# Optimization experiments

Hardware: AMD Instinct MI355X
Metric: run time of the kernel (lower is better)

The kernel has to match this reference:

```python
import jax, jax.numpy as jnp
import numpy as np

HIDDEN = 2048
HEADS = 16
HEAD_DIM = HIDDEN // HEADS  # 128
B, S = 2, 2048


def setup_inputs() -> dict:
    key = jax.random.key(0)
    ks = jax.random.split(key, 9)
    s_in = 1.0 / np.sqrt(HIDDEN)
    return {
        "X": jax.random.normal(ks[0], (B, S, HIDDEN), dtype=jnp.float32),
        "attention_mask": jnp.ones((B, S, S), dtype=jnp.int32),
        "Wq": jax.random.uniform(ks[1], (HIDDEN, HIDDEN), jnp.float32, -s_in, s_in),
        "bq": jax.random.uniform(ks[2], (HIDDEN,), jnp.float32, -s_in, s_in),
        "Wk": jax.random.uniform(ks[3], (HIDDEN, HEAD_DIM), jnp.float32, -s_in, s_in),
        "bk": jax.random.uniform(ks[4], (HEAD_DIM,), jnp.float32, -s_in, s_in),
        "Wv": jax.random.uniform(ks[5], (HIDDEN, HEAD_DIM), jnp.float32, -s_in, s_in),
        "bv": jax.random.uniform(ks[6], (HEAD_DIM,), jnp.float32, -s_in, s_in),
        "Wo": jax.random.uniform(ks[7], (HIDDEN, HIDDEN), jnp.float32, -s_in, s_in),
        "bo": jax.random.uniform(ks[8], (HIDDEN,), jnp.float32, -s_in, s_in),
    }


def reference(X, attention_mask, Wq, bq, Wk, bk, Wv, bv, Wo, bo):
    b, s, _ = X.shape
    # Projections
    Q = X @ Wq + bq                      # (B, S, H*D)
    K = X @ Wk + bk                      # (B, S, D)  shared across heads (MQA)
    V = X @ Wv + bv                      # (B, S, D)
    Q = Q.reshape(b, s, HEADS, HEAD_DIM).transpose(0, 2, 1, 3)  # (B, H, S, D)
    scale = 1.0 / jnp.sqrt(jnp.float32(HEAD_DIM))
    # QK^T with shared K head
    scores = jnp.einsum('bhqd,bkd->bhqk', Q, K) * scale          # (B, H, S, S)
    scores = jnp.where(attention_mask[:, None, :, :] == 0, -jnp.inf, scores)
    attn = jax.nn.softmax(scores, axis=-1)
    # dropout_rate = 0.0 (eval) -> identity
    out = jnp.einsum('bhqk,bkd->bhqd', attn, V)                  # (B, H, S, D)
    out = out.transpose(0, 2, 1, 3).reshape(b, s, HIDDEN)        # (B, S, hidden)
    return out @ Wo + bo
```

## Files before the change

### kernel.cpp

```cpp
#include <hip/hip_runtime.h>
#include <cstdint>
#include <cstddef>

#define HIDDEN 2048
#define HEADS 16
#define HD 128
#define BSZ 2
#define SEQ 2048
#define MTOT (BSZ * SEQ)
#define NQKV (HIDDEN + 2 * HD)
#define SL2E 0.12751743f

typedef unsigned short ushort_t;
typedef __attribute__((ext_vector_type(8))) __bf16 bf16x8;
typedef __attribute__((ext_vector_type(4))) float f32x4;

typedef __attribute__((address_space(3))) unsigned int as3_u32;
typedef __attribute__((address_space(1))) const unsigned int as1_u32;

__device__ __forceinline__ ushort_t f2bf(float x) {
  union { float f; unsigned u; } v; v.f = x;
  unsigned r = v.u + 0x7fffu + ((v.u >> 16) & 1u);
  return (ushort_t)(r >> 16);
}
__device__ __forceinline__ ushort_t f2bf_trunc(float x) {
  union { float f; unsigned u; } v; v.f = x;
  return (ushort_t)(v.u >> 16);
}

__device__ __forceinline__ void gld16(const void* g, void* lds) {
  __builtin_amdgcn_global_load_lds((as1_u32*)g, (as3_u32*)lds, 16, 0, 0);
}

__global__ __launch_bounds__(256) void cvt_bf16_kernel(
    const float* __restrict__ in, ushort_t* __restrict__ out, int n4) {
  int i = blockIdx.x * 256 + threadIdx.x;
  if (i >= n4) return;
  float4 v = ((const float4*)in)[i];
  ushort4 o;
  o.x = f2bf(v.x); o.y = f2bf(v.y); o.z = f2bf(v.z); o.w = f2bf(v.w);
  ((ushort4*)out)[i] = o;
}

__global__ __launch_bounds__(256) void cvtT_qkv_kernel(
    const float* __restrict__ Wq, const float* __restrict__ Wk,
    const float* __restrict__ Wv, ushort_t* __restrict__ WT) {
  __shared__ float tile[32][36];
  const int t = threadIdx.x;
  const int nb = blockIdx.x * 32, kb = blockIdx.y * 32;
  const float* W; int N, nc; float scale;
  if (nb < HIDDEN)            { W = Wq; N = HIDDEN; nc = nb;               scale = SL2E; }
  else if (nb < HIDDEN + HD)  { W = Wk; N = HD;     nc = nb - HIDDEN;      scale = 1.f; }
  else                        { W = Wv; N = HD;     nc = nb - HIDDEN - HD; scale = 1.f; }
  {
    int row = t >> 3, c4 = (t & 7) << 2;
    float4 v = *(const float4*)(W + (size_t)(kb + row) * N + nc + c4);
    tile[row][c4] = v.x * scale; tile[row][c4 + 1] = v.y * scale;
    tile[row][c4 + 2] = v.z * scale; tile[row][c4 + 3] = v.w * scale;
  }
  __syncthreads();
  {
    int nl = t >> 3, k4 = (t & 7) << 2;
    ushort4 o;
    o.x = f2bf(tile[k4 + 0][nl]); o.y = f2bf(tile[k4 + 1][nl]);
    o.z = f2bf(tile[k4 + 2][nl]); o.w = f2bf(tile[k4 + 3][nl]);
    *(ushort4*)(WT + (size_t)(nb + nl) * HIDDEN + kb + k4) = o;
  }
}

__global__ __launch_bounds__(256) void cvtT_kernel(
    const float* __restrict__ W, ushort_t* __restrict__ WT, int K, int N) {
  __shared__ float tile[32][36];
  const int t = threadIdx.x;
  const int kb = blockIdx.y * 32, nb = blockIdx.x * 32;
  {
    int row = t >> 3, c4 = (t & 7) << 2;
    float4 v = *(const float4*)(W + (size_t)(kb + row) * N + nb + c4);
    tile[row][c4] = v.x; tile[row][c4 + 1] = v.y;
    tile[row][c4 + 2] = v.z; tile[row][c4 + 3] = v.w;
  }
  __syncthreads();
  {
    int nl = t >> 3, k4 = (t & 7) << 2;
    ushort4 o;
    o.x = f2bf(tile[k4 + 0][nl]); o.y = f2bf(tile[k4 + 1][nl]);
    o.z = f2bf(tile[k4 + 2][nl]); o.w = f2bf(tile[k4 + 3][nl]);
    *(ushort4*)(WT + (size_t)(nb + nl) * K + kb + k4) = o;
  }
}

__global__ __launch_bounds__(256) void transpose_v_kernel(
    const ushort_t* __restrict__ Vin, ushort_t* __restrict__ Vt) {
  __shared__ ushort_t tile[32][40];
  const int t = threadIdx.x;
  const int rb = blockIdx.x * 32, cb = blockIdx.y * 32;
  {
    int row = t >> 3, c4 = (t & 7) << 2;
    ushort4 v = *(const ushort4*)(Vin + (size_t)(rb + row) * NQKV + cb + c4);
    tile[row][c4] = v.x; tile[row][c4 + 1] = v.y;
    tile[row][c4 + 2] = v.z; tile[row][c4 + 3] = v.w;
  }
  __syncthreads();
  {
    int dl = t >> 3, r4 = (t & 7) << 2;
    ushort4 o;
    o.x = tile[r4 + 0][dl]; o.y = tile[r4 + 1][dl];
    o.z = tile[r4 + 2][dl]; o.w = tile[r4 + 3][dl];
    *(ushort4*)(Vt + (size_t)(cb + dl) * MTOT + rb + r4) = o;
  }
}

__global__ void concat_bias_kernel(const float* __restrict__ bq,
                                   const float* __restrict__ bk,
                                   const float* __restrict__ bv,
                                   float* __restrict__ o) {
  int i = blockIdx.x * 256 + threadIdx.x;
  if (i >= NQKV) return;
  o[i] = (i < HIDDEN) ? bq[i] * SL2E
       : (i < HIDDEN + HD ? bk[i - HIDDEN] : bv[i - HIDDEN - HD]);
}

__global__ __launch_bounds__(256) void mask_flags_kernel(
    const int* __restrict__ mask, int* __restrict__ flags) {
  const int kt = blockIdx.x, qt = blockIdx.y, b = blockIdx.z;
  const int t = threadIdx.x;
  int allv = 1, anyv = 0;
  const size_t base = (size_t)b * SEQ * SEQ + (size_t)qt * 128 * SEQ + kt * 64;
  for (int i = t; i < 2048; i += 256) {
    const int row = i >> 4, c4 = (i & 15) << 2;
    const int4 v = *(const int4*)(mask + base + (size_t)row * SEQ + c4);
    const int nz = (v.x != 0) & (v.y != 0) & (v.z != 0) & (v.w != 0);
    const int nzany = (v.x != 0) | (v.y != 0) | (v.z != 0) | (v.w != 0);
    allv &= nz; anyv |= nzany;
  }
  const int wAll = __all(allv), wAny = __any(anyv);
  __shared__ int sA[4], sO[4];
  if ((t & 63) == 0) { sA[t >> 6] = wAll; sO[t >> 6] = wAny; }
  __syncthreads();
  if (t == 0) {
    const int A = sA[0] & sA[1] & sA[2] & sA[3];
    const int O = sO[0] | sO[1] | sO[2] | sO[3];
    flags[(b * 16 + qt) * 32 + kt] = A ? 2 : (O ? 1 : 0);
  }
}

template <int OUTF32>
__global__ __launch_bounds__(256) void gemm_mfma(
    const ushort_t* __restrict__ A, const ushort_t* __restrict__ Bt,
    const float* __restrict__ bias, void* __restrict__ C,
    int M, int N, int K, int nm_per_xcd) {
  __shared__ ushort_t As[2][128 * 64];
  __shared__ ushort_t Bs[2][128 * 64];
  const int t = threadIdx.x;
  const int w = t >> 6, l = t & 63;
  const int id = blockIdx.x;
  const int xcd = id & 7, j = id >> 3;
  const int mt = xcd * nm_per_xcd + (j % nm_per_xcd);
  const int nt = j / nm_per_xcd;
  const int mb = mt * 128, nb = nt * 128;
  const int wm = (w >> 1) * 64, wn = (w & 1) * 64;
  const int fl = l & 15, g = l >> 4;
  const int srow = l >> 3, cphys = l & 7;

  f32x4 acc[4][4];
#pragma unroll
  for (int i = 0; i < 4; ++i)
#pragma unroll
    for (int jj = 0; jj < 4; ++jj) acc[i][jj] = (f32x4){0.f, 0.f, 0.f, 0.f};

#pragma unroll
  for (int jj = 0; jj < 4; ++jj) {
    const int inst = w * 4 + jj;
    const int row = inst * 8 + srow;
    const int clog = cphys ^ (row & 7);
    gld16(A + (size_t)(mb + row) * K + clog * 8, &As[0][inst * 512]);
    gld16(Bt + (size_t)(nb + row) * K + clog * 8, &Bs[0][inst * 512]);
  }

  int cur = 0;
  for (int k0 = 0; k0 < K; k0 += 64) {
    __syncthreads();
    if (k0 + 64 < K) {
#pragma unroll
      for (int jj = 0; jj < 4; ++jj) {
        const int inst = w * 4 + jj;
        const int row = inst * 8 + srow;
        const int clog = cphys ^ (row & 7);
        gld16(A + (size_t)(mb + row) * K + k0 + 64 + clog * 8,
              &As[cur ^ 1][inst * 512]);
        gld16(Bt + (size_t)(nb + row) * K + k0 + 64 + clog * 8,
              &Bs[cur ^ 1][inst * 512]);
      }
    }
    const ushort_t* Ac = &As[cur][0];
    const ushort_t* Bc = &Bs[cur][0];
#pragma unroll
    for (int s = 0; s < 2; ++s) {
      bf16x8 af[4], bfr[4];
#pragma unroll
      for (int i = 0; i < 4; ++i) {
        const int m = wm + i * 16 + fl;
        af[i] = *(const bf16x8*)&Ac[m * 64 + (((s << 2) + g) ^ (m & 7)) * 8];
        const int n = wn + i * 16 + fl;
        bfr[i] = *(const bf16x8*)&Bc[n * 64 + (((s << 2) + g) ^ (n & 7)) * 8];
      }
#pragma unroll
      for (int i = 0; i < 4; ++i)
#pragma unroll
        for (int jj = 0; jj < 4; ++jj)
          acc[i][jj] = __builtin_amdgcn_mfma_f32_16x16x32_bf16(
              af[i], bfr[jj], acc[i][jj], 0, 0, 0);
    }
    cur ^= 1;
  }

#pragma unroll
  for (int jj = 0; jj < 4; ++jj) {
    const int col = nb + wn + jj * 16 + fl;
    const float bv = bias[col];
#pragma unroll
    for (int i = 0; i < 4; ++i) {
      const int row0 = mb + wm + i * 16 + g * 4;
#pragma unroll
      for (int r = 0; r < 4; ++r) {
        const float val = acc[i][jj][r] + bv;
        if (OUTF32)
          ((float*)C)[(size_t)(row0 + r) * N + col] = val;
        else
          ((ushort_t*)C)[(size_t)(row0 + r) * N + col] = f2bf(val);
      }
    }
  }
}

__global__ __launch_bounds__(256, 2) void flash_mfma(
    const ushort_t* __restrict__ QKV,
    const ushort_t* __restrict__ Vt,
    const int* __restrict__ mask,
    const int* __restrict__ flags,
    ushort_t* __restrict__ Ab)
{
  __shared__ ushort_t Kbuf[2][64 * 128];
  __shared__ ushort_t Vbuf[2][128 * 64];
  __shared__ ushort_t Ps[128 * 64];

  const int qt = blockIdx.x, h = blockIdx.y, b = blockIdx.z;
  const int t = threadIdx.x, w = t >> 6, l = t & 63;
  const int fl = l & 15, g = l >> 4;
  const int qbase = qt * 128;

  bf16x8 qf[2][4];
#pragma unroll
  for (int im = 0; im < 2; ++im) {
    const int qrow = qbase + w * 32 + im * 16 + fl;
#pragma unroll
    for (int ks = 0; ks < 4; ++ks)
      qf[im][ks] = *(const bf16x8*)(QKV + (size_t)(b * SEQ + qrow) * NQKV +
                                    h * HD + ks * 32 + g * 8);
  }

  bf16x8 onesf;
  {
    const ushort_t ov = (fl == 0) ? (ushort_t)0x3F80 : (ushort_t)0;
#pragma unroll
    for (int jj = 0; jj < 8; ++jj) ((ushort_t*)&onesf)[jj] = ov;
  }

#pragma unroll
  for (int j = 0; j < 4; ++j) {
    const int inst = w * 4 + j;
    const int krow = inst * 4 + (l >> 4);
    const int ck = (l & 15) ^ (krow & 15);
    gld16(QKV + (size_t)(b * SEQ + krow) * NQKV + HIDDEN + ck * 8,
          &Kbuf[0][inst * 512]);
    const int drow = inst * 8 + (l >> 3);
    const int cv = (l & 7) ^ (drow & 7);
    gld16(Vt + (size_t)drow * MTOT + b * SEQ + cv * 8, &Vbuf[0][inst * 512]);
  }

  const size_t mbase = (size_t)b * SEQ * SEQ;
  const int qrowc0 = qbase + w * 32 + g * 4;

  f32x4 oacc[2][9];
#pragma unroll
  for (int im = 0; im < 2; ++im)
#pragma unroll
    for (int d = 0; d < 9; ++d) oacc[im][d] = (f32x4){0.f, 0.f, 0.f, 0.f};

  int cur = 0;
  for (int kt = 0; kt < SEQ / 64; ++kt) {
    const int kbase = kt * 64;
    const int flag = flags[((b * 16 + qt) << 5) + kt];
    __syncthreads();

    {
      const int knb = (kt + 1 < SEQ / 64) ? (kbase + 64) : kbase;
#pragma unroll
      for (int j = 0; j < 4; ++j) {
        const int inst = w * 4 + j;
        const int krow = inst * 4 + (l >> 4);
        const int ck = (l & 15) ^ (krow & 15);
        gld16(QKV + (size_t)(b * SEQ + knb + krow) * NQKV + HIDDEN + ck * 8,
              &Kbuf[cur ^ 1][inst * 512]);
        const int drow = inst * 8 + (l >> 3);
        const int cv = (l & 7) ^ (drow & 7);
        gld16(Vt + (size_t)drow * MTOT + b * SEQ + knb + cv * 8,
              &Vbuf[cur ^ 1][inst * 512]);
      }
    }

    const ushort_t* Kc = &Kbuf[cur][0];
    f32x4 sc[2][4];
#pragma unroll
    for (int im = 0; im < 2; ++im)
#pragma unroll
      for (int ct = 0; ct < 4; ++ct) sc[im][ct] = (f32x4){0.f, 0.f, 0.f, 0.f};
#pragma unroll
    for (int ks = 0; ks < 4; ++ks) {
#pragma unroll
      for (int ct = 0; ct < 4; ++ct) {
        const int key = ct * 16 + fl;
        const bf16x8 kf =
            *(const bf16x8*)&Kc[key * 128 + ((ks * 4 + g) ^ (key & 15)) * 8];
        sc[0][ct] = __builtin_amdgcn_mfma_f32_16x16x32_bf16(qf[0][ks], kf,
                                                            sc[0][ct], 0, 0, 0);
        sc[1][ct] = __builtin_amdgcn_mfma_f32_16x16x32_bf16(qf[1][ks], kf,
                                                            sc[1][ct], 0, 0, 0);
      }
    }

    if (flag != 2) {
#pragma unroll
      for (int im = 0; im < 2; ++im) {
        const int qrc = qrowc0 + im * 16;
#pragma unroll
        for (int ct = 0; ct < 4; ++ct)
#pragma unroll
          for (int r = 0; r < 4; ++r) {
            const int mv =
                mask[mbase + (size_t)(qrc + r) * SEQ + kbase + ct * 16 + fl];
            if (!mv) sc[im][ct][r] = -1e30f;
          }
      }
    }

#pragma unroll
    for (int im = 0; im < 2; ++im)
#pragma unroll
      for (int ct = 0; ct < 4; ++ct)
#pragma unroll
        for (int r = 0; r < 4; ++r) {
          const float p = __builtin_amdgcn_exp2f(sc[im][ct][r]);
          const int row = w * 32 + im * 16 + g * 4 + r;
          Ps[row * 64 + (((ct << 1) + (fl >> 3)) ^ (row & 7)) * 8 + (fl & 7)] =
              f2bf_trunc(p);
        }

    bf16x8 pf[2][2];
#pragma unroll
    for (int im = 0; im < 2; ++im) {
      const int prow = w * 32 + im * 16 + fl;
#pragma unroll
      for (int ks = 0; ks < 2; ++ks)
        pf[im][ks] = *(const bf16x8*)&Ps[prow * 64 +
                                         (((ks << 2) + g) ^ (fl & 7)) * 8];
    }

    const ushort_t* Vc = &Vbuf[cur][0];
#pragma unroll
    for (int dt = 0; dt < 8; ++dt) {
      const int drow = dt * 16 + fl;
#pragma unroll
      for (int ks = 0; ks < 2; ++ks) {
        const bf16x8 vf =
            *(const bf16x8*)&Vc[drow * 64 + ((ks * 4 + g) ^ (drow & 7)) * 8];
        oacc[0][dt] = __builtin_amdgcn_mfma_f32_16x16x32_bf16(pf[0][ks], vf,
                                                              oacc[0][dt], 0, 0, 0);
        oacc[1][dt] = __builtin_amdgcn_mfma_f32_16x16x32_bf16(pf[1][ks], vf,
                                                              oacc[1][dt], 0, 0, 0);
      }
    }
#pragma unroll
    for (int ks = 0; ks < 2; ++ks) {
      oacc[0][8] = __builtin_amdgcn_mfma_f32_16x16x32_bf16(pf[0][ks], onesf,
                                                           oacc[0][8], 0, 0, 0);
      oacc[1][8] = __builtin_amdgcn_mfma_f32_16x16x32_bf16(pf[1][ks], onesf,
                                                           oacc[1][8], 0, 0, 0);
    }
    cur ^= 1;
  }

#pragma unroll
  for (int im = 0; im < 2; ++im) {
#pragma unroll
    for (int r = 0; r < 4; ++r) {
      const float lsum = __shfl(oacc[im][8][r], (l & 48), 64);
      const float invl = 1.0f / lsum;
      const int row = b * SEQ + qrowc0 + im * 16 + r;
#pragma unroll
      for (int dt = 0; dt < 8; ++dt) {
        const int col = h * HD + dt * 16 + fl;
        Ab[(size_t)row * HIDDEN + col] = f2bf(oacc[im][dt][r] * invl);
      }
    }
  }
}

extern "C" void kernel_launch(void* const* d_in, const int* in_sizes, int n_in,
                              void* d_out, int out_size, void* d_ws, size_t ws_size,
                              hipStream_t stream) {
  const float* X  = (const float*)d_in[0];
  const int* mask = (const int*)d_in[1];
  const float* Wq = (const float*)d_in[2];
  const float* bq = (const float*)d_in[3];
  const float* Wk = (const float*)d_in[4];
  const float* bk = (const float*)d_in[5];
  const float* Wv = (const float*)d_in[6];
  const float* bv = (const float*)d_in[7];
  const float* Wo = (const float*)d_in[8];
  const float* bo = (const float*)d_in[9];
  float* out = (float*)d_out;

  char* p = (char*)d_ws;
  ushort_t* QKVb = (ushort_t*)p; p += (size_t)MTOT * NQKV * 2;
  ushort_t* Xb   = (ushort_t*)p; p += (size_t)MTOT * HIDDEN * 2;
  ushort_t* WT   = (ushort_t*)p; p += (size_t)NQKV * HIDDEN * 2;
  ushort_t* WoT  = (ushort_t*)p; p += (size_t)HIDDEN * HIDDEN * 2;
  ushort_t* Vt   = (ushort_t*)p; p += (size_t)HD * MTOT * 2;
  float* biasQKV = (float*)p;    p += 4096;
  int* flags     = (int*)p;      p += BSZ * 16 * 32 * 4;
  ushort_t* Ab = Xb;

  cvt_bf16_kernel<<<(MTOT * HIDDEN / 4 + 255) / 256, 256, 0, stream>>>(
      X, Xb, MTOT * HIDDEN / 4);
  cvtT_qkv_kernel<<<dim3(NQKV / 32, HIDDEN / 32), 256, 0, stream>>>(
      Wq, Wk, Wv, WT);
  cvtT_kernel<<<dim3(HIDDEN / 32, HIDDEN / 32), 256, 0, stream>>>(
      Wo, WoT, HIDDEN, HIDDEN);
  concat_bias_kernel<<<(NQKV + 255) / 256, 256, 0, stream>>>(bq, bk, bv, biasQKV);
  mask_flags_kernel<<<dim3(32, 16, BSZ), 256, 0, stream>>>(mask, flags);

  gemm_mfma<0><<<dim3((MTOT / 128) * (NQKV / 128)), 256, 0, stream>>>(
      Xb, WT, biasQKV, QKVb, MTOT, NQKV, HIDDEN, (MTOT / 128) / 8);
  transpose_v_kernel<<<dim3(MTOT / 32, HD / 32), 256, 0, stream>>>(
      QKVb + HIDDEN + HD, Vt);
  flash_mfma<<<dim3(SEQ / 128, HEADS, BSZ), 256, 0, stream>>>(
      QKVb, Vt, mask, flags, Ab);
  gemm_mfma<1><<<dim3((MTOT / 128) * (HIDDEN / 128)), 256, 0, stream>>>(
      Ab, WoT, bo, out, MTOT, HIDDEN, HIDDEN, (MTOT / 128) / 8);
}
```

Before: 343.8 us.

## Switch flash attention to 32x32x16 MFMA with register-resident P via permlane swap

Rewrites the flash attention inner loop to use 32x32x16 bf16 MFMA tiles. S is computed transposed (K as the A operand), so the exponentiated probabilities can be packed and redistributed across lanes with v_permlane32_swap instead of round-tripping through a shared-memory P buffer. The Ps LDS array and its write/read traffic are removed, the row-sum ones-trick becomes a single 32x32 accumulator, and s_setprio is raised around the MFMA blocks. The change also alters the mask access pattern and register pressure, which may affect occupancy.

```diff
diff --git a/kernel.cpp b/kernel.cpp
--- a/kernel.cpp
+++ b/kernel.cpp
@@ -14,6 +14,7 @@
 typedef unsigned short ushort_t;
 typedef __attribute__((ext_vector_type(8))) __bf16 bf16x8;
 typedef __attribute__((ext_vector_type(4))) float f32x4;
+typedef __attribute__((ext_vector_type(16))) float f32x16;
 
 typedef __attribute__((address_space(3))) unsigned int as3_u32;
 typedef __attribute__((address_space(1))) const unsigned int as1_u32;
@@ -23,9 +24,9 @@
   unsigned r = v.u + 0x7fffu + ((v.u >> 16) & 1u);
   return (ushort_t)(r >> 16);
 }
-__device__ __forceinline__ ushort_t f2bf_trunc(float x) {
-  union { float f; unsigned u; } v; v.f = x;
-  return (ushort_t)(v.u >> 16);
+__device__ __forceinline__ unsigned pk_bf16(float a, float b) {
+  union { float f; unsigned u; } x, y; x.f = a; y.f = b;
+  return (x.u >> 16) | (y.u & 0xFFFF0000u);
 }
 
 __device__ __forceinline__ void gld16(const void* g, void* lds) {
@@ -242,26 +243,22 @@
 {
   __shared__ ushort_t Kbuf[2][64 * 128];
   __shared__ ushort_t Vbuf[2][128 * 64];
-  __shared__ ushort_t Ps[128 * 64];
 
   const int qt = blockIdx.x, h = blockIdx.y, b = blockIdx.z;
   const int t = threadIdx.x, w = t >> 6, l = t & 63;
-  const int fl = l & 15, g = l >> 4;
+  const int q31 = l & 31, hi = l >> 5;
   const int qbase = qt * 128;
-
-  bf16x8 qf[2][4];
-#pragma unroll
-  for (int im = 0; im < 2; ++im) {
-    const int qrow = qbase + w * 32 + im * 16 + fl;
-#pragma unroll
-    for (int ks = 0; ks < 4; ++ks)
-      qf[im][ks] = *(const bf16x8*)(QKV + (size_t)(b * SEQ + qrow) * NQKV +
-                                    h * HD + ks * 32 + g * 8);
-  }
+  const int qrow = qbase + w * 32 + q31;
+
+  bf16x8 qf[8];
+#pragma unroll
+  for (int ks = 0; ks < 8; ++ks)
+    qf[ks] = *(const bf16x8*)(QKV + (size_t)(b * SEQ + qrow) * NQKV + h * HD +
+                              ks * 16 + hi * 8);
 
   bf16x8 onesf;
   {
-    const ushort_t ov = (fl == 0) ? (ushort_t)0x3F80 : (ushort_t)0;
+    const ushort_t ov = (q31 == 0) ? (ushort_t)0x3F80 : (ushort_t)0;
 #pragma unroll
     for (int jj = 0; jj < 8; ++jj) ((ushort_t*)&onesf)[jj] = ov;
   }
@@ -279,13 +276,14 @@
   }
 
   const size_t mbase = (size_t)b * SEQ * SEQ;
-  const int qrowc0 = qbase + w * 32 + g * 4;
-
-  f32x4 oacc[2][9];
-#pragma unroll
-  for (int im = 0; im < 2; ++im)
-#pragma unroll
-    for (int d = 0; d < 9; ++d) oacc[im][d] = (f32x4){0.f, 0.f, 0.f, 0.f};
+
+  f32x16 oacc[4], lacc;
+#pragma unroll
+  for (int d = 0; d < 4; ++d)
+#pragma unroll
+    for (int r = 0; r < 16; ++r) oacc[d][r] = 0.f;
+#pragma unroll
+  for (int r = 0; r < 16; ++r) lacc[r] = 0.f;
 
   int cur = 0;
   for (int kt = 0; kt < SEQ / 64; ++kt) {
@@ -310,99 +308,85 @@
     }
 
     const ushort_t* Kc = &Kbuf[cur][0];
-    f32x4 sc[2][4];
-#pragma unroll
-    for (int im = 0; im < 2; ++im)
-#pragma unroll
-      for (int ct = 0; ct < 4; ++ct) sc[im][ct] = (f32x4){0.f, 0.f, 0.f, 0.f};
+    f32x16 sc[2];
+#pragma unroll
+    for (int kk = 0; kk < 2; ++kk)
+#pragma unroll
+      for (int r = 0; r < 16; ++r) sc[kk][r] = 0.f;
+
+    __builtin_amdgcn_s_setprio(1);
+#pragma unroll
+    for (int ks = 0; ks < 8; ++ks)
+#pragma unroll
+      for (int kk = 0; kk < 2; ++kk) {
+        const int key = kk * 32 + q31;
+        const bf16x8 kf = *(const bf16x8*)&Kc[key * 128 +
+                                              (((ks << 1) + hi) ^ (key & 15)) * 8];
+        sc[kk] = __builtin_amdgcn_mfma_f32_32x32x16_bf16(kf, qf[ks], sc[kk],
+                                                         0, 0, 0);
+      }
+    __builtin_amdgcn_s_setprio(0);
+
+    if (flag != 2) {
+#pragma unroll
+      for (int kk = 0; kk < 2; ++kk)
+#pragma unroll
+        for (int r = 0; r < 16; ++r) {
+          const int key = kbase + kk * 32 + (r & 3) + ((r >> 2) << 3) + (hi << 2);
+          if (!mask[mbase + (size_t)qrow * SEQ + key]) sc[kk][r] = -1e30f;
+        }
+    }
+
+    bf16x8 pa[4];
+#pragma unroll
+    for (int kk = 0; kk < 2; ++kk) {
+      float pv[16];
+#pragma unroll
+      for (int r = 0; r < 16; ++r) pv[r] = __builtin_amdgcn_exp2f(sc[kk][r]);
+#pragma unroll
+      for (int half = 0; half < 2; ++half) {
+        const int bs = half * 8;
+        unsigned a0 = pk_bf16(pv[bs + 0], pv[bs + 1]);
+        unsigned a1 = pk_bf16(pv[bs + 2], pv[bs + 3]);
+        unsigned b0 = pk_bf16(pv[bs + 4], pv[bs + 5]);
+        unsigned b1 = pk_bf16(pv[bs + 6], pv[bs + 7]);
+        asm("v_permlane32_swap_b32 %0, %1" : "+v"(a0), "+v"(b0));
+        asm("v_permlane32_swap_b32 %0, %1" : "+v"(a1), "+v"(b1));
+        union { unsigned u[4]; bf16x8 v; } uu;
+        uu.u[0] = a0; uu.u[1] = a1; uu.u[2] = b0; uu.u[3] = b1;
+        pa[kk * 2 + half] = uu.v;
+      }
+    }
+
+    const ushort_t* Vc = &Vbuf[cur][0];
+    __builtin_amdgcn_s_setprio(1);
 #pragma unroll
     for (int ks = 0; ks < 4; ++ks) {
 #pragma unroll
-      for (int ct = 0; ct < 4; ++ct) {
-        const int key = ct * 16 + fl;
-        const bf16x8 kf =
-            *(const bf16x8*)&Kc[key * 128 + ((ks * 4 + g) ^ (key & 15)) * 8];
-        sc[0][ct] = __builtin_amdgcn_mfma_f32_16x16x32_bf16(qf[0][ks], kf,
-                                                            sc[0][ct], 0, 0, 0);
-        sc[1][ct] = __builtin_amdgcn_mfma_f32_16x16x32_bf16(qf[1][ks], kf,
-                                                            sc[1][ct], 0, 0, 0);
-      }
-    }
-
-    if (flag != 2) {
-#pragma unroll
-      for (int im = 0; im < 2; ++im) {
-        const int qrc = qrowc0 + im * 16;
-#pragma unroll
-        for (int ct = 0; ct < 4; ++ct)
-#pragma unroll
-          for (int r = 0; r < 4; ++r) {
-            const int mv =
-                mask[mbase + (size_t)(qrc + r) * SEQ + kbase + ct * 16 + fl];
-            if (!mv) sc[im][ct][r] = -1e30f;
-          }
-      }
-    }
-
-#pragma unroll
-    for (int im = 0; im < 2; ++im)
-#pragma unroll
-      for (int ct = 0; ct < 4; ++ct)
-#pragma unroll
-        for (int r = 0; r < 4; ++r) {
-          const float p = __builtin_amdgcn_exp2f(sc[im][ct][r]);
-          const int row = w * 32 + im * 16 + g * 4 + r;
-          Ps[row * 64 + (((ct << 1) + (fl >> 3)) ^ (row & 7)) * 8 + (fl & 7)] =
-              f2bf_trunc(p);
-        }
-
-    bf16x8 pf[2][2];
-#pragma unroll
-    for (int im = 0; im < 2; ++im) {
-      const int prow = w * 32 + im * 16 + fl;
-#pragma unroll
-      for (int ks = 0; ks < 2; ++ks)
-        pf[im][ks] = *(const bf16x8*)&Ps[prow * 64 +
-                                         (((ks << 2) + g) ^ (fl & 7)) * 8];
-    }
-
-    const ushort_t* Vc = &Vbuf[cur][0];
-#pragma unroll
-    for (int dt = 0; dt < 8; ++dt) {
-      const int drow = dt * 16 + fl;
-#pragma unroll
-      for (int ks = 0; ks < 2; ++ks) {
-        const bf16x8 vf =
-            *(const bf16x8*)&Vc[drow * 64 + ((ks * 4 + g) ^ (drow & 7)) * 8];
-        oacc[0][dt] = __builtin_amdgcn_mfma_f32_16x16x32_bf16(pf[0][ks], vf,
-                                                              oacc[0][dt], 0, 0, 0);
-        oacc[1][dt] = __builtin_amdgcn_mfma_f32_16x16x32_bf16(pf[1][ks], vf,
-                                                              oacc[1][dt], 0, 0, 0);
-      }
-    }
-#pragma unroll
-    for (int ks = 0; ks < 2; ++ks) {
-      oacc[0][8] = __builtin_amdgcn_mfma_f32_16x16x32_bf16(pf[0][ks], onesf,
-                                                           oacc[0][8], 0, 0, 0);
-      oacc[1][8] = __builtin_amdgcn_mfma_f32_16x16x32_bf16(pf[1][ks], onesf,
-                                                           oacc[1][8], 0, 0, 0);
-    }
+      for (int dt = 0; dt < 4; ++dt) {
+        const int d = dt * 32 + q31;
+        const bf16x8 vf = *(const bf16x8*)&Vc[d * 64 +
+                                              (((ks << 1) + hi) ^ (d & 7)) * 8];
+        oacc[dt] = __builtin_amdgcn_mfma_f32_32x32x16_bf16(pa[ks], vf,
+                                                           oacc[dt], 0, 0, 0);
+      }
+      lacc = __builtin_amdgcn_mfma_f32_32x32x16_bf16(pa[ks], onesf, lacc,
+                                                     0, 0, 0);
+    }
+    __builtin_amdgcn_s_setprio(0);
     cur ^= 1;
   }
 
 #pragma unroll
-  for (int im = 0; im < 2; ++im) {
-#pragma unroll
-    for (int r = 0; r < 4; ++r) {
-      const float lsum = __shfl(oacc[im][8][r], (l & 48), 64);
-      const float invl = 1.0f / lsum;
-      const int row = b * SEQ + qrowc0 + im * 16 + r;
-#pragma unroll
-      for (int dt = 0; dt < 8; ++dt) {
-        const int col = h * HD + dt * 16 + fl;
-        Ab[(size_t)row * HIDDEN + col] = f2bf(oacc[im][dt][r] * invl);
-      }
-    }
+  for (int r = 0; r < 16; ++r) {
+    const float ls = __shfl(lacc[r], l & 32, 64);
+    const float invl = 1.0f / ls;
+    const int row = b * SEQ + qbase + w * 32 + (r & 3) + ((r >> 2) << 3) +
+                    (hi << 2);
+#pragma unroll
+    for (int dt = 0; dt < 4; ++dt)
+      Ab[(size_t)row * HIDDEN + h * HD + dt * 32 + q31] =
+          f2bf(oacc[dt][r] * invl);
   }
 }
 
```

After: 340.2 us. No clear change (-1.0%).
